# Optimization experiments

Hardware: AMD Instinct MI355X
Metric: run time of the kernel (lower is better)

The kernel has to match this reference:

```python
import jax, jax.numpy as jnp
import numpy as np
import math

B, S, D, H = 4, 2048, 1024, 16
AD = D // H  # per-head dim = 64
EPS = 1e-5


def setup_inputs() -> dict:
    key = jax.random.key(0)
    ks = jax.random.split(key, 13)
    s = lambda fan_in: 1.0 / math.sqrt(fan_in)
    return {
        "x": jax.random.normal(ks[0], (B, S, D), dtype=jnp.float32),
        "ln1_w": jnp.ones((D,), jnp.float32),
        "ln1_b": jnp.zeros((D,), jnp.float32),
        "ln2_w": jnp.ones((D,), jnp.float32),
        "ln2_b": jnp.zeros((D,), jnp.float32),
        "W_qkv": jax.random.uniform(ks[1], (D, 3 * D), jnp.float32, -s(D), s(D)),
        "b_qkv": jax.random.uniform(ks[2], (3 * D,), jnp.float32, -s(D), s(D)),
        "W_o": jax.random.uniform(ks[3], (D, D), jnp.float32, -s(D), s(D)),
        "b_o": jax.random.uniform(ks[4], (D,), jnp.float32, -s(D), s(D)),
        "W_up": jax.random.uniform(ks[5], (D, 4 * D), jnp.float32, -s(D), s(D)),
        "b_up": jax.random.uniform(ks[6], (4 * D,), jnp.float32, -s(D), s(D)),
        "W_down": jax.random.uniform(ks[7], (4 * D, D), jnp.float32, -s(4 * D), s(4 * D)),
        "b_down": jax.random.uniform(ks[8], (D,), jnp.float32, -s(4 * D), s(4 * D)),
    }


def _layernorm(x, w, b):
    mu = jnp.mean(x, axis=-1, keepdims=True)
    var = jnp.mean(jnp.square(x - mu), axis=-1, keepdims=True)
    return (x - mu) * jax.lax.rsqrt(var + EPS) * w + b


def reference(x, ln1_w, ln1_b, ln2_w, ln2_b, W_qkv, b_qkv, W_o, b_o,
              W_up, b_up, W_down, b_down):
    b, s, d = x.shape
    # --- pre-norm attention ---
    xn = _layernorm(x, ln1_w, ln1_b)
    qkv = (xn @ W_qkv + b_qkv).reshape(b, s, H, 3, AD)
    q = qkv[:, :, :, 0, :]  # [b,s,h,ad]
    k = qkv[:, :, :, 1, :]
    v = qkv[:, :, :, 2, :]
    scores = jnp.einsum("bqhd,bkhd->bhqk", q, k) / math.sqrt(AD)
    causal = jnp.tril(jnp.ones((s, s), dtype=bool))  # True = keep
    scores = jnp.where(causal, scores, -jnp.inf)
    attn = jax.nn.softmax(scores, axis=-1)
    ctx = jnp.einsum("bhqk,bkhd->bqhd", attn, v).reshape(b, s, d)
    attn_out = ctx @ W_o + b_o + x
    # --- pre-norm MLP (gelu, exact erf as in torch GELU) ---
    hn = _layernorm(attn_out, ln2_w, ln2_b)
    h = jax.nn.gelu(hn @ W_up + b_up, approximate=False)
    return h @ W_down + b_down + attn_out
```

## Files before the change

kernel.cpp:

```cpp
#include <hip/hip_runtime.h>
#include <hip/hip_bf16.h>
#include <math.h>

#define S_LEN 2048
#define DMODEL 1024
#define NHEAD 16
#define HDIM 64

typedef __attribute__((ext_vector_type(8))) short bf16x8;
typedef __attribute__((ext_vector_type(4))) float f32x4;
typedef __attribute__((ext_vector_type(8))) unsigned short u16x8;

#define GLOAD_LDS16(g, l)                                                      \
  __builtin_amdgcn_global_load_lds(                                            \
      (const __attribute__((address_space(1))) void*)(g),                      \
      (__attribute__((address_space(3))) void*)(l), 16, 0, 0)

static __device__ __forceinline__ unsigned short f2bf(float f) {
  union { float f; unsigned int i; } u; u.f = f;
  unsigned int r = u.i + 0x7fff + ((u.i >> 16) & 1);
  return (unsigned short)(r >> 16);
}

__global__ __launch_bounds__(256) void wtrans_kernel(const float* __restrict__ W,
                                                     unsigned short* __restrict__ Wt,
                                                     int K, int N) {
  __shared__ float tile[32][33];
  int tx = threadIdx.x, ty = threadIdx.y;
  int n0 = blockIdx.x * 32, k0 = blockIdx.y * 32;
#pragma unroll
  for (int i = 0; i < 4; ++i)
    tile[ty * 4 + i][tx] = W[(size_t)(k0 + ty * 4 + i) * N + n0 + tx];
  __syncthreads();
#pragma unroll
  for (int i = 0; i < 4; ++i)
    Wt[(size_t)(n0 + ty * 4 + i) * K + k0 + tx] = f2bf(tile[tx][ty * 4 + i]);
}

__global__ __launch_bounds__(256) void ln_kernel(const float* __restrict__ X,
                                                 const float* __restrict__ w,
                                                 const float* __restrict__ b,
                                                 unsigned short* __restrict__ out) {
  int row = blockIdx.x;
  int t = threadIdx.x;
  const float4* xr = (const float4*)(X + (size_t)row * DMODEL);
  float4 v = xr[t];
  float s = v.x + v.y + v.z + v.w;
  float q = v.x * v.x + v.y * v.y + v.z * v.z + v.w * v.w;
#pragma unroll
  for (int m = 1; m < 64; m <<= 1) {
    s += __shfl_xor(s, m, 64);
    q += __shfl_xor(q, m, 64);
  }
  __shared__ float red[8];
  int wv = t >> 6;
  if ((t & 63) == 0) { red[wv] = s; red[4 + wv] = q; }
  __syncthreads();
  s = red[0] + red[1] + red[2] + red[3];
  q = red[4] + red[5] + red[6] + red[7];
  float mu = s * (1.0f / DMODEL);
  float var = q * (1.0f / DMODEL) - mu * mu;
  float rs = rsqrtf(var + 1e-5f);
  float4 wv4 = ((const float4*)w)[t];
  float4 bv4 = ((const float4*)b)[t];
  ushort4 o;
  o.x = f2bf((v.x - mu) * rs * wv4.x + bv4.x);
  o.y = f2bf((v.y - mu) * rs * wv4.y + bv4.y);
  o.z = f2bf((v.z - mu) * rs * wv4.z + bv4.z);
  o.w = f2bf((v.w - mu) * rs * wv4.w + bv4.w);
  ((ushort4*)(out + (size_t)row * DMODEL))[t] = o;
}

template <int EPI>
__global__ __launch_bounds__(256) void gemm_kernel(
    const unsigned short* __restrict__ A, const unsigned short* __restrict__ Bt,
    const float* __restrict__ bias, int N, int K,
    void* __restrict__ o0, void* __restrict__ o1, void* __restrict__ o2,
    const float* __restrict__ extra) {
  __shared__ __align__(16) unsigned short sA[128 * 32];
  __shared__ __align__(16) unsigned short sB[128 * 32];
  const int t = threadIdx.x;
  const int w = t >> 6, lane = t & 63;
  const int wr = w >> 1, wc = w & 1;

  const int gx = gridDim.x;
  const int nwg = gx * gridDim.y;
  int bid = blockIdx.y * gx + blockIdx.x;
  {
    int xcd = bid & 7, pos = bid >> 3;
    int qq = nwg >> 3, rr = nwg & 7;
    bid = (xcd < rr ? xcd * (qq + 1) : rr * (qq + 1) + (xcd - rr) * qq) + pos;
  }
  const int m0 = (bid / gx) * 128, n0 = (bid % gx) * 128;

  const int o0b = w * 2048 + lane * 16;
  const int o1b = o0b + 1024;
  const char* gA0 = (const char*)A + (size_t)(m0 + (o0b >> 6)) * K * 2 + (o0b & 63);
  const char* gA1 = (const char*)A + (size_t)(m0 + (o1b >> 6)) * K * 2 + (o1b & 63);
  const char* gB0 = (const char*)Bt + (size_t)(n0 + (o0b >> 6)) * K * 2 + (o0b & 63);
  const char* gB1 = (const char*)Bt + (size_t)(n0 + (o1b >> 6)) * K * 2 + (o1b & 63);
  char* lA = (char*)sA + w * 2048;
  char* lB = (char*)sB + w * 2048;

  f32x4 acc[4][4] = {};
  const int lc = lane & 15, lh = lane >> 4;
  const int aoff = (wr * 64 + lc) * 32 + lh * 8;
  const int boff = (wc * 64 + lc) * 32 + lh * 8;

  for (int k0 = 0; k0 < K; k0 += 32) {
    __syncthreads();
    GLOAD_LDS16(gA0 + (size_t)k0 * 2, lA);
    GLOAD_LDS16(gA1 + (size_t)k0 * 2, lA + 1024);
    GLOAD_LDS16(gB0 + (size_t)k0 * 2, lB);
    GLOAD_LDS16(gB1 + (size_t)k0 * 2, lB + 1024);
    __syncthreads();
    bf16x8 af[4], bg[4];
#pragma unroll
    for (int i = 0; i < 4; ++i) af[i] = *(const bf16x8*)(sA + aoff + i * 16 * 32);
#pragma unroll
    for (int i = 0; i < 4; ++i) bg[i] = *(const bf16x8*)(sB + boff + i * 16 * 32);
#pragma unroll
    for (int i = 0; i < 4; ++i)
#pragma unroll
      for (int j = 0; j < 4; ++j)
        acc[i][j] = __builtin_amdgcn_mfma_f32_16x16x32_bf16(af[i], bg[j], acc[i][j], 0, 0, 0);
  }

#pragma unroll
  for (int i = 0; i < 4; ++i)
#pragma unroll
    for (int j = 0; j < 4; ++j) {
      int col = n0 + wc * 64 + j * 16 + lc;
      float bcol = bias[col];
#pragma unroll
      for (int r = 0; r < 4; ++r) {
        int row = m0 + wr * 64 + i * 16 + lh * 4 + r;
        float val = acc[i][j][r] + bcol;
        if constexpr (EPI == 0) {
          int bb = row >> 11, srow = row & 2047;
          int hh = col / 192, rem = col - hh * 192;
          int which = rem >> 6, a = rem & 63;
          unsigned short* dst =
              which == 0 ? (unsigned short*)o0 : which == 1 ? (unsigned short*)o1 : (unsigned short*)o2;
          dst[(((size_t)bb * NHEAD + hh) * S_LEN + srow) * HDIM + a] = f2bf(val);
        } else if constexpr (EPI == 2) {
          float g = 0.5f * val * (1.0f + erff(val * 0.70710678118654752f));
          ((unsigned short*)o0)[(size_t)row * N + col] = f2bf(g);
        } else {
          size_t idx = (size_t)row * DMODEL + col;
          ((float*)o0)[idx] = val + extra[idx];
        }
      }
    }
}

__global__ __launch_bounds__(256) void attn_kernel(
    const unsigned short* __restrict__ Q, const unsigned short* __restrict__ Kk,
    const unsigned short* __restrict__ V, unsigned short* __restrict__ ctx) {
  __shared__ __align__(16) unsigned short sK[64 * 64];
  __shared__ __align__(16) unsigned short sVt[64 * 72];
  __shared__ __align__(16) unsigned short sP[4][16 * 72];

  const int pi = blockIdx.x;
  const int bh = blockIdx.y;
  const int t = threadIdx.x;
  const int w = t >> 6, lane = t & 63;
  const int lc = lane & 15, lh = lane >> 4;
  const int qtA = pi, qtB = 31 - pi;
  const size_t base = (size_t)bh * S_LEN * HDIM;
  const unsigned short* Qb = Q + base;
  const unsigned short* Kb = Kk + base;
  const unsigned short* Vb = V + base;

  bf16x8 qfA[2], qfB[2];
  {
    const unsigned short* qa = Qb + (size_t)(qtA * 64 + w * 16 + lc) * HDIM;
    const unsigned short* qb = Qb + (size_t)(qtB * 64 + w * 16 + lc) * HDIM;
    qfA[0] = *(const bf16x8*)(qa + lh * 8);
    qfA[1] = *(const bf16x8*)(qa + 32 + lh * 8);
    qfB[0] = *(const bf16x8*)(qb + lh * 8);
    qfB[1] = *(const bf16x8*)(qb + 32 + lh * 8);
  }

  f32x4 accA[4] = {}, accB[4] = {};
  float mA[4], lA[4], mB[4], lB[4];
#pragma unroll
  for (int r = 0; r < 4; ++r) { mA[r] = -INFINITY; lA[r] = 0.f; mB[r] = -INFINITY; lB[r] = 0.f; }

  const float SCL = 0.125f * 1.44269504088896f;

  auto process = [&](const bf16x8 (&qf)[2], f32x4 (&acc)[4], float (&mrow)[4],
                     float (&lrow)[4], bool diag) {
    f32x4 s[4] = {};
    __builtin_amdgcn_s_setprio(1);
#pragma unroll
    for (int f = 0; f < 4; ++f) {
      int row = f * 16 + lc;
      int swz = (row & 7) << 4;
#pragma unroll
      for (int kk = 0; kk < 2; ++kk) {
        int cb = kk * 64 + lh * 16;
        bf16x8 kf = *(const bf16x8*)((const char*)sK + row * 128 + (cb ^ swz));
        s[f] = __builtin_amdgcn_mfma_f32_16x16x32_bf16(qf[kk], kf, s[f], 0, 0, 0);
      }
    }
    __builtin_amdgcn_s_setprio(0);
#pragma unroll
    for (int f = 0; f < 4; ++f)
#pragma unroll
      for (int r = 0; r < 4; ++r) {
        float sv = s[f][r] * SCL;
        if (diag && (f * 16 + lc > w * 16 + lh * 4 + r)) sv = -INFINITY;
        s[f][r] = sv;
      }
    float alpha[4];
#pragma unroll
    for (int r = 0; r < 4; ++r) {
      float mv = fmaxf(fmaxf(s[0][r], s[1][r]), fmaxf(s[2][r], s[3][r]));
#pragma unroll
      for (int msk = 1; msk < 16; msk <<= 1) mv = fmaxf(mv, __shfl_xor(mv, msk, 64));
      float mnew = fmaxf(mrow[r], mv);
      alpha[r] = __builtin_amdgcn_exp2f(mrow[r] - mnew);
      mrow[r] = mnew;
    }
#pragma unroll
    for (int r = 0; r < 4; ++r) {
      float ps = 0.f;
#pragma unroll
      for (int f = 0; f < 4; ++f) {
        float p = __builtin_amdgcn_exp2f(s[f][r] - mrow[r]);
        s[f][r] = p;
        ps += p;
      }
#pragma unroll
      for (int msk = 1; msk < 16; msk <<= 1) ps += __shfl_xor(ps, msk, 64);
      lrow[r] = lrow[r] * alpha[r] + ps;
#pragma unroll
      for (int f = 0; f < 4; ++f) acc[f][r] *= alpha[r];
    }
    unsigned short* Pw = &sP[w][0];
#pragma unroll
    for (int f = 0; f < 4; ++f)
#pragma unroll
      for (int r = 0; r < 4; ++r)
        Pw[(lh * 4 + r) * 72 + f * 16 + lc] = f2bf(s[f][r]);
    bf16x8 pa[2];
#pragma unroll
    for (int kk = 0; kk < 2; ++kk)
      pa[kk] = *(const bf16x8*)(Pw + lc * 72 + kk * 32 + lh * 8);
    __builtin_amdgcn_s_setprio(1);
#pragma unroll
    for (int f = 0; f < 4; ++f)
#pragma unroll
      for (int kk = 0; kk < 2; ++kk) {
        bf16x8 bv = *(const bf16x8*)(sVt + (f * 16 + lc) * 72 + kk * 32 + lh * 8);
        acc[f] = __builtin_amdgcn_mfma_f32_16x16x32_bf16(pa[kk], bv, acc[f], 0, 0, 0);
      }
    __builtin_amdgcn_s_setprio(0);
  };

  for (int tile = 0; tile <= qtB; ++tile) {
    const int kv0 = tile * 64;
    __syncthreads();
    {
      const char* Ks = (const char*)(Kb + (size_t)kv0 * HDIM);
#pragma unroll
      for (int c = 0; c < 2; ++c) {
        int o = w * 2048 + c * 1024 + lane * 16;
        int row = o >> 7, cb = o & 127;
        int cbs = cb ^ ((row & 7) << 4);
        GLOAD_LDS16(Ks + row * 128 + cbs, (char*)sK + w * 2048 + c * 1024);
      }
    }
    {
      const unsigned short* Vs = Vb + (size_t)kv0 * HDIM;
      const int d0 = w * 16;
      u16x8 v0 = *(const u16x8*)(Vs + (size_t)lane * HDIM + d0);
      u16x8 v1 = *(const u16x8*)(Vs + (size_t)lane * HDIM + d0 + 8);
#pragma unroll
      for (int j = 0; j < 8; ++j) sVt[(d0 + j) * 72 + lane] = (unsigned short)v0[j];
#pragma unroll
      for (int j = 0; j < 8; ++j) sVt[(d0 + 8 + j) * 72 + lane] = (unsigned short)v1[j];
    }
    __syncthreads();

    process(qfB, accB, mB, lB, tile == qtB);
    if (tile <= qtA) process(qfA, accA, mA, lA, tile == qtA);
  }

  const int b = bh >> 4, h = bh & 15;
  auto writeout = [&](int qt, f32x4 (&acc)[4], float (&lrow)[4]) {
#pragma unroll
    for (int r = 0; r < 4; ++r) {
      float inv = 1.0f / lrow[r];
      int qg = qt * 64 + w * 16 + lh * 4 + r;
#pragma unroll
      for (int f = 0; f < 4; ++f)
        ctx[((size_t)b * S_LEN + qg) * DMODEL + h * HDIM + f * 16 + lc] = f2bf(acc[f][r] * inv);
    }
  };
  writeout(qtA, accA, lA);
  writeout(qtB, accB, lB);
}

extern "C" void kernel_launch(void* const* d_in, const int* in_sizes, int n_in,
                              void* d_out, int out_size, void* d_ws, size_t ws_size,
                              hipStream_t stream) {
  const float* x    = (const float*)d_in[0];
  const float* ln1w = (const float*)d_in[1];
  const float* ln1b = (const float*)d_in[2];
  const float* ln2w = (const float*)d_in[3];
  const float* ln2b = (const float*)d_in[4];
  const float* Wqkv = (const float*)d_in[5];
  const float* bqkv = (const float*)d_in[6];
  const float* Wo   = (const float*)d_in[7];
  const float* bo   = (const float*)d_in[8];
  const float* Wup  = (const float*)d_in[9];
  const float* bup  = (const float*)d_in[10];
  const float* Wdn  = (const float*)d_in[11];
  const float* bdn  = (const float*)d_in[12];

  char* ws = (char*)d_ws;
  unsigned short* xn  = (unsigned short*)(ws + 0);
  unsigned short* qb  = (unsigned short*)(ws + 16777216);
  unsigned short* kb  = (unsigned short*)(ws + 33554432);
  unsigned short* vb  = (unsigned short*)(ws + 50331648);
  unsigned short* hb  = (unsigned short*)(ws + 0);
  unsigned short* ctx = (unsigned short*)(ws + 67108864);
  unsigned short* hn  = (unsigned short*)(ws + 67108864);
  float* attn         = (float*)(ws + 83886080);
  unsigned short* WtQKV = (unsigned short*)(ws + 117440512);
  unsigned short* WtO   = (unsigned short*)(ws + 123731968);
  unsigned short* WtUP  = (unsigned short*)(ws + 125829120);
  unsigned short* WtDN  = (unsigned short*)(ws + 134217728);

  dim3 tb(32, 8);
  wtrans_kernel<<<dim3(3072 / 32, 1024 / 32), tb, 0, stream>>>(Wqkv, WtQKV, 1024, 3072);
  wtrans_kernel<<<dim3(1024 / 32, 1024 / 32), tb, 0, stream>>>(Wo, WtO, 1024, 1024);
  wtrans_kernel<<<dim3(4096 / 32, 1024 / 32), tb, 0, stream>>>(Wup, WtUP, 1024, 4096);
  wtrans_kernel<<<dim3(1024 / 32, 4096 / 32), tb, 0, stream>>>(Wdn, WtDN, 4096, 1024);

  ln_kernel<<<8192, 256, 0, stream>>>(x, ln1w, ln1b, xn);

  gemm_kernel<0><<<dim3(3072 / 128, 8192 / 128), 256, 0, stream>>>(
      xn, WtQKV, bqkv, 3072, 1024, qb, kb, vb, nullptr);

  attn_kernel<<<dim3(16, 64), 256, 0, stream>>>(qb, kb, vb, ctx);

  gemm_kernel<1><<<dim3(1024 / 128, 8192 / 128), 256, 0, stream>>>(
      ctx, WtO, bo, 1024, 1024, attn, nullptr, nullptr, x);

  ln_kernel<<<8192, 256, 0, stream>>>(attn, ln2w, ln2b, hn);

  gemm_kernel<2><<<dim3(4096 / 128, 8192 / 128), 256, 0, stream>>>(
      hn, WtUP, bup, 4096, 1024, hb, nullptr, nullptr, nullptr);

  gemm_kernel<3><<<dim3(1024 / 128, 8192 / 128), 256, 0, stream>>>(
      hb, WtDN, bdn, 1024, 4096, d_out, nullptr, nullptr, attn);
}
```

Before: 628.6 us.

## Add 256x256-tile double-buffered GEMM for QKV and up-projection

Adds a new 512-thread GEMM kernel with 256x256 output tiles and BK=64. It uses double-buffered LDS filled by direct global-to-LDS loads with an XOR swizzle, interleaves the staging of the next k-tile across four compute phases, and raises wave priority around the MFMA blocks. The QKV and up-projection GEMMs move to this kernel to get more data reuse per tile and to overlap loads with compute. The older 128-tile kernel stays only for the residual-add GEMMs. In exchange, the new kernel uses 128KB of LDS and launches fewer workgroups, which can reduce occupancy and leave fewer tiles to balance across CUs.

```diff
diff --git a/kernel.cpp b/kernel.cpp
--- a/kernel.cpp
+++ b/kernel.cpp
@@ -72,11 +72,124 @@
 }
 
 template <int EPI>
+__global__ __launch_bounds__(512, 2) void gemm256_kernel(
+    const unsigned short* __restrict__ A, const unsigned short* __restrict__ Bt,
+    const float* __restrict__ bias, int N, int K,
+    void* __restrict__ o0, void* __restrict__ o1, void* __restrict__ o2) {
+  __shared__ __align__(16) unsigned short lds[2][2][2][128 * 64];
+  const int t = threadIdx.x;
+  const int w = t >> 6, lane = t & 63;
+  const int qr = w >> 2, qc = w & 3;
+  const int lc = lane & 15, lh = lane >> 4;
+
+  const int gx = gridDim.x;
+  const int nwg = gx * gridDim.y;
+  int bid = blockIdx.y * gx + blockIdx.x;
+  {
+    int xcd = bid & 7, pos = bid >> 3;
+    int qq = nwg >> 3, rr = nwg & 7;
+    bid = (xcd < rr ? xcd * (qq + 1) : rr * (qq + 1) + (xcd - rr) * qq) + pos;
+  }
+  const int m0 = (bid / gx) * 256, n0 = (bid % gx) * 256;
+
+  const int srow = lane >> 3;
+  const int scol = 16 * ((lane & 7) ^ srow);
+  const size_t ld2 = (size_t)K * 2;
+  const char* gA = (const char*)A + (size_t)(m0 + 16 * w + srow) * ld2 + scol;
+  const char* gB = (const char*)Bt + (size_t)(n0 + 16 * w + srow) * ld2 + scol;
+  const int ldsw = w * 1024;
+
+  f32x4 acc[4][8] = {};
+
+  const int sw = (lc & 7) << 4;
+  const int NT = K >> 6;
+
+  auto stage_half = [&](int buf, int mat, int half, int kt) {
+    const char* g = (mat == 0 ? gA : gB) + (size_t)half * 128 * ld2 + (size_t)kt * 128;
+    unsigned short* l = &lds[buf][mat][half][ldsw];
+    GLOAD_LDS16(g, l);
+    GLOAD_LDS16(g + 8 * ld2, (char*)l + 1024);
+  };
+
+  stage_half(0, 0, 0, 0);
+  stage_half(0, 1, 0, 0);
+  stage_half(0, 1, 1, 0);
+  stage_half(0, 0, 1, 0);
+  asm volatile("s_waitcnt vmcnt(4)" ::: "memory");
+  __builtin_amdgcn_s_barrier();
+
+  for (int kt = 0; kt < NT; ++kt) {
+    const int cur = kt & 1;
+    const int nkt = (kt + 1 < NT) ? kt + 1 : kt;
+#pragma unroll
+    for (int ph = 0; ph < 4; ++ph) {
+      const int mh = ph >> 1, nh = ph & 1;
+      const unsigned short* ha = lds[cur][0][mh];
+      const unsigned short* hb = lds[cur][1][nh];
+      bf16x8 af[2][4], bf[2][2];
+#pragma unroll
+      for (int ks = 0; ks < 2; ++ks) {
+        const int cc = ((ks << 6) | (lh << 4)) ^ sw;
+#pragma unroll
+        for (int fm = 0; fm < 4; ++fm)
+          af[ks][fm] = *(const bf16x8*)((const char*)ha + (qr * 64 + fm * 16 + lc) * 128 + cc);
+#pragma unroll
+        for (int fn = 0; fn < 2; ++fn)
+          bf[ks][fn] = *(const bf16x8*)((const char*)hb + (qc * 32 + fn * 16 + lc) * 128 + cc);
+      }
+      const int smat = (ph == 0 || ph == 3) ? 0 : 1;
+      const int shalf = (ph >= 2) ? 1 : 0;
+      stage_half(cur ^ 1, smat, shalf, nkt);
+      __builtin_amdgcn_s_barrier();
+      __builtin_amdgcn_s_setprio(1);
+#pragma unroll
+      for (int ks = 0; ks < 2; ++ks)
+#pragma unroll
+        for (int fm = 0; fm < 4; ++fm)
+#pragma unroll
+          for (int fn = 0; fn < 2; ++fn)
+            acc[ph][fm * 2 + fn] = __builtin_amdgcn_mfma_f32_16x16x32_bf16(
+                af[ks][fm], bf[ks][fn], acc[ph][fm * 2 + fn], 0, 0, 0);
+      __builtin_amdgcn_s_setprio(0);
+      if (ph != 2) asm volatile("s_waitcnt vmcnt(4)" ::: "memory");
+      __builtin_amdgcn_s_barrier();
+    }
+  }
+
+#pragma unroll
+  for (int q = 0; q < 4; ++q) {
+    const int mh = q >> 1, nh = q & 1;
+#pragma unroll
+    for (int fm = 0; fm < 4; ++fm)
+#pragma unroll
+      for (int fn = 0; fn < 2; ++fn) {
+        int col = n0 + nh * 128 + qc * 32 + fn * 16 + lc;
+        float bcol = bias[col];
+#pragma unroll
+        for (int r = 0; r < 4; ++r) {
+          int row = m0 + mh * 128 + qr * 64 + fm * 16 + lh * 4 + r;
+          float val = acc[q][fm * 2 + fn][r] + bcol;
+          if constexpr (EPI == 0) {
+            int bb = row >> 11, srw = row & 2047;
+            int hh = col / 192, rem = col - hh * 192;
+            int which = rem >> 6, a = rem & 63;
+            unsigned short* dst =
+                which == 0 ? (unsigned short*)o0 : which == 1 ? (unsigned short*)o1 : (unsigned short*)o2;
+            dst[(((size_t)bb * NHEAD + hh) * S_LEN + srw) * HDIM + a] = f2bf(val);
+          } else {
+            float g = 0.5f * val * (1.0f + erff(val * 0.70710678118654752f));
+            ((unsigned short*)o0)[(size_t)row * N + col] = f2bf(g);
+          }
+        }
+      }
+  }
+}
+
+template <int EPI>
 __global__ __launch_bounds__(256) void gemm_kernel(
     const unsigned short* __restrict__ A, const unsigned short* __restrict__ Bt,
     const float* __restrict__ bias, int N, int K,
-    void* __restrict__ o0, void* __restrict__ o1, void* __restrict__ o2,
-    const float* __restrict__ extra) {
+    void* __restrict__ o0, const float* __restrict__ extra) {
   __shared__ __align__(16) unsigned short sA[128 * 32];
   __shared__ __align__(16) unsigned short sB[128 * 32];
   const int t = threadIdx.x;
@@ -136,20 +249,8 @@
       for (int r = 0; r < 4; ++r) {
         int row = m0 + wr * 64 + i * 16 + lh * 4 + r;
         float val = acc[i][j][r] + bcol;
-        if constexpr (EPI == 0) {
-          int bb = row >> 11, srow = row & 2047;
-          int hh = col / 192, rem = col - hh * 192;
-          int which = rem >> 6, a = rem & 63;
-          unsigned short* dst =
-              which == 0 ? (unsigned short*)o0 : which == 1 ? (unsigned short*)o1 : (unsigned short*)o2;
-          dst[(((size_t)bb * NHEAD + hh) * S_LEN + srow) * HDIM + a] = f2bf(val);
-        } else if constexpr (EPI == 2) {
-          float g = 0.5f * val * (1.0f + erff(val * 0.70710678118654752f));
-          ((unsigned short*)o0)[(size_t)row * N + col] = f2bf(g);
-        } else {
-          size_t idx = (size_t)row * DMODEL + col;
-          ((float*)o0)[idx] = val + extra[idx];
-        }
+        size_t idx = (size_t)row * DMODEL + col;
+        ((float*)o0)[idx] = val + extra[idx];
       }
     }
 }
@@ -342,19 +443,19 @@
 
   ln_kernel<<<8192, 256, 0, stream>>>(x, ln1w, ln1b, xn);
 
-  gemm_kernel<0><<<dim3(3072 / 128, 8192 / 128), 256, 0, stream>>>(
-      xn, WtQKV, bqkv, 3072, 1024, qb, kb, vb, nullptr);
+  gemm256_kernel<0><<<dim3(3072 / 256, 8192 / 256), 512, 0, stream>>>(
+      xn, WtQKV, bqkv, 3072, 1024, qb, kb, vb);
 
   attn_kernel<<<dim3(16, 64), 256, 0, stream>>>(qb, kb, vb, ctx);
 
   gemm_kernel<1><<<dim3(1024 / 128, 8192 / 128), 256, 0, stream>>>(
-      ctx, WtO, bo, 1024, 1024, attn, nullptr, nullptr, x);
+      ctx, WtO, bo, 1024, 1024, attn, x);
 
   ln_kernel<<<8192, 256, 0, stream>>>(attn, ln2w, ln2b, hn);
 
-  gemm_kernel<2><<<dim3(4096 / 128, 8192 / 128), 256, 0, stream>>>(
-      hn, WtUP, bup, 4096, 1024, hb, nullptr, nullptr, nullptr);
+  gemm256_kernel<2><<<dim3(4096 / 256, 8192 / 256), 512, 0, stream>>>(
+      hn, WtUP, bup, 4096, 1024, hb, nullptr, nullptr);
 
   gemm_kernel<3><<<dim3(1024 / 128, 8192 / 128), 256, 0, stream>>>(
-      hb, WtDN, bdn, 1024, 4096, d_out, nullptr, nullptr, attn);
-}
+      hb, WtDN, bdn, 1024, 4096, d_out, attn);
+}
```

Measured after the change: 615.2 us. 2.1% less time.
